# Kernel optimization log

Hardware: AMD Instinct MI355X
Metric: run time of the kernel (lower is better)

The kernel has to match this reference:

```python
import jax, jax.numpy as jnp
import numpy as np

K = 512
D = 512
N_D = 4
SUB_D = D // N_D  # 128
B, T = 16, 2048
TAU = 2.0


def setup_inputs() -> dict:
    key = jax.random.key(0)
    kx, kw1, kw2, kw3, kw4, kg = jax.random.split(key, 6)
    x = jax.random.normal(kx, (B, D, T), dtype=jnp.float32)
    scale = 1.0 / K
    def init_w(k):
        return jax.random.uniform(k, (K, SUB_D), dtype=jnp.float32, minval=-scale, maxval=scale)
    W1, W2, W3, W4 = init_w(kw1), init_w(kw2), init_w(kw3), init_w(kw4)
    # Standard Gumbel noise g = -log(-log(U)), fixed here for reproducibility
    u = jax.random.uniform(kg, (N_D, B * T, K), dtype=jnp.float32, minval=1e-10, maxval=1.0)
    gumbels = -jnp.log(-jnp.log(u))
    return {"x": x, "W1": W1, "W2": W2, "W3": W3, "W4": W4, "gumbels": gumbels}


def reference(x, W1, W2, W3, W4, gumbels):
    # x: [B, D, T] -> [B, T, D] -> flat [N, D] -> [n_d, N, sub_D]
    Bv, Dv, Tv = x.shape
    flat = jnp.transpose(x, (0, 2, 1)).reshape(-1, Dv)          # [N, D]
    xg = jnp.transpose(flat.reshape(-1, N_D, SUB_D), (1, 0, 2))  # [n_d, N, sub_D]
    W = jnp.stack([W1, W2, W3, W4], axis=0)                      # [n_d, K, sub_D]

    code_sqr = jnp.sum(W * W, axis=-1)                           # [n_d, K]
    in_sqr = jnp.sum(xg * xg, axis=-1, keepdims=True)            # [n_d, N, 1]
    cross = jnp.einsum('gnd,gkd->gnk', xg, W)                    # [n_d, N, K]
    dis = code_sqr[:, None, :] + in_sqr - 2.0 * cross            # [n_d, N, K]

    # gumbel_softmax(-dis, tau, hard=False): softmax((logits + g)/tau)
    enc = jax.nn.softmax((-dis + gumbels) / TAU, axis=-1)        # [n_d, N, K]

    quant = jnp.einsum('gnk,gkd->gnd', enc, W)                   # [n_d, N, sub_D]
    quant = jnp.transpose(quant, (1, 0, 2)).reshape(Bv, Tv, Dv)  # concat sub-dims
    quant = jnp.transpose(quant, (0, 2, 1))                      # [B, D, T]

    avg_probs = jnp.mean(enc, axis=1)                            # [n_d, K]
    perp = jnp.sum(jnp.exp(-jnp.sum(avg_probs * jnp.log(avg_probs + 1e-10), axis=-1)))
    return quant, perp
```

## Files before the change

### kernel.cpp

```cpp
#include <hip/hip_runtime.h>
#include <hip/hip_bf16.h>
#include <math.h>

#define K_CODES 512
#define D_FULL 512
#define SUB_D 128
#define N_D 4
#define B_SZ 16
#define T_SZ 2048
#define N_TOK (B_SZ * T_SZ)
#define TILE 32
#define XS_STRIDE 136
#define ENC_STRIDE 520
#define QS_STRIDE 33

typedef __attribute__((ext_vector_type(8))) short short8;
typedef __attribute__((ext_vector_type(16))) float f32x16;

__device__ __forceinline__ unsigned short f2bf(float f) {
    __hip_bfloat16 h = __float2bfloat16(f);
    return *reinterpret_cast<unsigned short*>(&h);
}
__device__ __forceinline__ float bf2f(unsigned short u) {
    unsigned int v = ((unsigned int)u) << 16;
    return __uint_as_float(v);
}

#define XS_OFF  33280
#define RED_OFF 41984
#define SMEM_SZ 42496

__global__ __launch_bounds__(256, 3) void vq_kernel(
    const float* __restrict__ x,
    const unsigned short* __restrict__ Wbf,
    const unsigned short* __restrict__ WTbf,
    const float* __restrict__ csqr,
    const float* __restrict__ gum,
    float* __restrict__ out,
    float* __restrict__ wsum, int Rmask)
{
    __shared__ __align__(16) char smem[SMEM_SZ];
    unsigned short* enc = (unsigned short*)smem;
    unsigned short* xs  = (unsigned short*)(smem + XS_OFF);
    float* Sred = (float*)(smem + RED_OFF);
    float* Qs   = (float*)smem;

    const int tid = threadIdx.x;
    const int g = blockIdx.y;
    const int n0 = blockIdx.x * TILE;
    const int b = n0 / T_SZ;
    const int t0 = n0 % T_SZ;
    const int wave = tid >> 6, lane = tid & 63;
    const int half = lane >> 5, l31 = lane & 31;

    const float* xbase = x + ((size_t)b * D_FULL + g * SUB_D) * T_SZ + t0;
    #pragma unroll
    for (int it = 0; it < 4; ++it) {
        int idx = tid + it * 256;
        int tq = idx & 7, d = idx >> 3;
        float4 v = *(const float4*)(xbase + (size_t)d * T_SZ + tq * 4);
        int t = tq * 4;
        xs[(t + 0) * XS_STRIDE + d] = f2bf(v.x);
        xs[(t + 1) * XS_STRIDE + d] = f2bf(v.y);
        xs[(t + 2) * XS_STRIDE + d] = f2bf(v.z);
        xs[(t + 3) * XS_STRIDE + d] = f2bf(v.w);
    }
    __syncthreads();

    short8 afrag[8];
    #pragma unroll
    for (int s = 0; s < 8; ++s)
        afrag[s] = *(const short8*)(xs + l31 * XS_STRIDE + s * 16 + half * 8);

    float csq[4];
    #pragma unroll
    for (int ct = 0; ct < 4; ++ct)
        csq[ct] = csqr[g * K_CODES + wave * 128 + ct * 32 + l31];

    __syncthreads();

    const unsigned short* Wg = Wbf + (size_t)g * K_CODES * SUB_D;
    f32x16 acc[4];
    #pragma unroll
    for (int ct = 0; ct < 4; ++ct)
        #pragma unroll
        for (int i = 0; i < 16; ++i) acc[ct][i] = 0.f;

    #pragma unroll
    for (int s = 0; s < 8; ++s) {
        #pragma unroll
        for (int ct = 0; ct < 4; ++ct) {
            short8 bfrag = *(const short8*)(Wg + (size_t)(wave * 128 + ct * 32 + l31) * SUB_D
                                            + s * 16 + half * 8);
            acc[ct] = __builtin_amdgcn_mfma_f32_32x32x16_bf16(afrag[s], bfrag, acc[ct], 0, 0, 0);
        }
    }

    __builtin_amdgcn_sched_barrier(0);

    const float* gw = gum + ((size_t)g * N_TOK + n0) * K_CODES + wave * 128;
    float4 f[16];
    #pragma unroll
    for (int k = 0; k < 16; ++k)
        f[k] = *(const float4*)(gw + (size_t)(2 * k + half) * K_CODES + 4 * l31);

    float* Sw = (float*)(smem + XS_OFF) + wave * 544;
    float ssum[16];
    #pragma unroll
    for (int i = 0; i < 16; ++i) ssum[i] = 0.f;

    #pragma unroll
    for (int j = 0; j < 8; ++j) {
        *(float4*)(Sw + half * 128 + 4 * l31)       = f[2 * j];
        *(float4*)(Sw + 256 + half * 128 + 4 * l31) = f[2 * j + 1];
        int hj = j & 1;
        if (half == hj) {
            int q = (j - hj) >> 1;
            #pragma unroll
            for (int ct = 0; ct < 4; ++ct)
                #pragma unroll
                for (int m = 0; m < 4; ++m) {
                    float gv = Sw[m * 128 + ct * 32 + l31];
                    int i = q * 4 + m;
                    float e = __expf(acc[ct][i] - 0.5f * csq[ct] + 0.5f * gv);
                    acc[ct][i] = e;
                    ssum[i] += e;
                }
        }
    }

    #pragma unroll
    for (int i = 0; i < 16; ++i) {
        float s = ssum[i];
        s += __shfl_xor(s, 1);  s += __shfl_xor(s, 2);
        s += __shfl_xor(s, 4);  s += __shfl_xor(s, 8);
        s += __shfl_xor(s, 16);
        ssum[i] = s;
    }
    if (l31 == 0) {
        #pragma unroll
        for (int i = 0; i < 16; ++i)
            Sred[((i & 3) + 8 * (i >> 2) + 4 * half) * 4 + wave] = ssum[i];
    }
    __syncthreads();
    float rinv[16];
    #pragma unroll
    for (int i = 0; i < 16; ++i) {
        int r = (i & 3) + 8 * (i >> 2) + 4 * half;
        float4 sv = *(const float4*)&Sred[r * 4];
        rinv[i] = 1.f / (sv.x + sv.y + sv.z + sv.w);
    }

    float* wrep = wsum + (size_t)(blockIdx.x & Rmask) * (N_D * K_CODES) + g * K_CODES;
    #pragma unroll
    for (int ct = 0; ct < 4; ++ct) {
        float s = 0.f;
        #pragma unroll
        for (int i = 0; i < 16; ++i) {
            int r = (i & 3) + 8 * (i >> 2) + 4 * half;
            float p = acc[ct][i] * rinv[i];
            enc[r * ENC_STRIDE + wave * 128 + ct * 32 + l31] = f2bf(p);
            s += p;
        }
        s += __shfl_xor(s, 32);
        if (half == 0) atomicAdd(wrep + wave * 128 + ct * 32 + l31, s);
    }
    __syncthreads();

    const unsigned short* Btrow = WTbf + (size_t)g * SUB_D * K_CODES
                                + (size_t)(wave * 32 + l31) * K_CODES + half * 8;
    f32x16 q0, q1;
    #pragma unroll
    for (int i = 0; i < 16; ++i) { q0[i] = 0.f; q1[i] = 0.f; }
    #pragma unroll
    for (int s = 0; s < 32; s += 2) {
        short8 a0 = *(const short8*)(enc + l31 * ENC_STRIDE + (s + 0) * 16 + half * 8);
        short8 b0 = *(const short8*)(Btrow + (s + 0) * 16);
        short8 a1 = *(const short8*)(enc + l31 * ENC_STRIDE + (s + 1) * 16 + half * 8);
        short8 b1 = *(const short8*)(Btrow + (s + 1) * 16);
        q0 = __builtin_amdgcn_mfma_f32_32x32x16_bf16(a0, b0, q0, 0, 0, 0);
        q1 = __builtin_amdgcn_mfma_f32_32x32x16_bf16(a1, b1, q1, 0, 0, 0);
    }
    __syncthreads();

    #pragma unroll
    for (int i = 0; i < 16; ++i) {
        int r = (i & 3) + 8 * (i >> 2) + 4 * half;
        Qs[(wave * 32 + l31) * QS_STRIDE + r] = q0[i] + q1[i];
    }
    __syncthreads();

    float* obase = out + ((size_t)b * D_FULL + g * SUB_D) * T_SZ + t0;
    #pragma unroll
    for (int it = 0; it < 4; ++it) {
        int idx = tid + it * 256;
        int t4 = (idx & 7) * 4, j = idx >> 3;
        float4 v;
        v.x = Qs[j * QS_STRIDE + t4 + 0];
        v.y = Qs[j * QS_STRIDE + t4 + 1];
        v.z = Qs[j * QS_STRIDE + t4 + 2];
        v.w = Qs[j * QS_STRIDE + t4 + 3];
        *(float4*)(obase + (size_t)j * T_SZ + t4) = v;
    }
}

__global__ __launch_bounds__(256) void prep_kernel(
    const float* __restrict__ W1, const float* __restrict__ W2,
    const float* __restrict__ W3, const float* __restrict__ W4,
    unsigned short* __restrict__ Wbf, unsigned short* __restrict__ WTbf,
    float* __restrict__ csqr)
{
    const int g = blockIdx.x, kc = blockIdx.y;
    const float* Wg = (g == 0) ? W1 : ((g == 1) ? W2 : ((g == 2) ? W3 : W4));
    const int tid = threadIdx.x;
    const int k0 = kc * 64;
    __shared__ float tile[64][129];

    #pragma unroll
    for (int it = 0; it < 8; ++it) {
        int idx = tid + it * 256;
        int k = idx >> 5, d4 = (idx & 31) * 4;
        float4 v = *(const float4*)(Wg + (size_t)(k0 + k) * SUB_D + d4);
        unsigned short p0 = f2bf(v.x), p1 = f2bf(v.y), p2 = f2bf(v.z), p3 = f2bf(v.w);
        tile[k][d4 + 0] = bf2f(p0); tile[k][d4 + 1] = bf2f(p1);
        tile[k][d4 + 2] = bf2f(p2); tile[k][d4 + 3] = bf2f(p3);
        ushort4 pk; pk.x = p0; pk.y = p1; pk.z = p2; pk.w = p3;
        *(ushort4*)(Wbf + (size_t)g * K_CODES * SUB_D + (size_t)(k0 + k) * SUB_D + d4) = pk;
    }
    __syncthreads();

    #pragma unroll
    for (int it = 0; it < 4; ++it) {
        int idx = tid + it * 256;
        int d = idx >> 3, c8 = (idx & 7) * 8;
        union { unsigned short u[8]; short8 v; } pk;
        #pragma unroll
        for (int j = 0; j < 8; ++j) pk.u[j] = f2bf(tile[c8 + j][d]);
        *(short8*)(WTbf + (size_t)g * SUB_D * K_CODES + (size_t)d * K_CODES + k0 + c8) = pk.v;
    }

    if (tid < 64) {
        float ssq = 0.f;
        #pragma unroll 16
        for (int d = 0; d < SUB_D; ++d) { float wv = tile[tid][d]; ssq += wv * wv; }
        csqr[g * K_CODES + k0 + tid] = ssq;
    }
}

__global__ __launch_bounds__(256) void perp_kernel(
    const float* __restrict__ wsum, int R, float* __restrict__ out)
{
    const int tid = threadIdx.x;
    const int lane = tid & 63, wave = tid >> 6;
    __shared__ float red[N_D][4];
    float part[N_D];
    #pragma unroll
    for (int g = 0; g < N_D; ++g) part[g] = 0.f;

    for (int g = 0; g < N_D; ++g) {
        for (int kk = tid; kk < K_CODES; kk += 256) {
            float s = 0.f;
            for (int r = 0; r < R; ++r) s += wsum[(size_t)r * (N_D * K_CODES) + g * K_CODES + kk];
            float p = s * (1.0f / N_TOK);
            part[g] += p * logf(p + 1e-10f);
        }
    }
    #pragma unroll
    for (int g = 0; g < N_D; ++g) {
        float v = part[g];
        #pragma unroll
        for (int off = 32; off; off >>= 1) v += __shfl_xor(v, off);
        if (lane == 0) red[g][wave] = v;
    }
    __syncthreads();
    if (tid == 0) {
        float perp = 0.f;
        #pragma unroll
        for (int g = 0; g < N_D; ++g) {
            float e = red[g][0] + red[g][1] + red[g][2] + red[g][3];
            perp += __expf(-e);
        }
        out[(size_t)B_SZ * D_FULL * T_SZ] = perp;
    }
}

extern "C" void kernel_launch(void* const* d_in, const int* in_sizes, int n_in,
                              void* d_out, int out_size, void* d_ws, size_t ws_size,
                              hipStream_t stream) {
    const float* x   = (const float*)d_in[0];
    const float* W1  = (const float*)d_in[1];
    const float* W2  = (const float*)d_in[2];
    const float* W3  = (const float*)d_in[3];
    const float* W4  = (const float*)d_in[4];
    const float* gum = (const float*)d_in[5];
    float* out = (float*)d_out;

    unsigned short* Wbf  = (unsigned short*)d_ws;
    unsigned short* WTbf = Wbf + (size_t)N_D * K_CODES * SUB_D;
    float* csqr = (float*)(WTbf + (size_t)N_D * K_CODES * SUB_D);
    float* wsum = csqr + N_D * K_CODES;

    size_t fixed = (size_t)N_D * K_CODES * SUB_D * 2 * 2 + (size_t)N_D * K_CODES * 4;
    size_t rem = (ws_size > fixed) ? (ws_size - fixed) : 0;
    int maxR = (int)(rem / ((size_t)N_D * K_CODES * 4));
    int R = 1;
    while (R * 2 <= maxR && R < 16) R *= 2;

    hipMemsetAsync(wsum, 0, (size_t)R * N_D * K_CODES * sizeof(float), stream);
    prep_kernel<<<dim3(4, 8), 256, 0, stream>>>(W1, W2, W3, W4, Wbf, WTbf, csqr);
    vq_kernel<<<dim3(N_TOK / TILE, N_D), 256, 0, stream>>>(x, Wbf, WTbf, csqr, gum, out, wsum, R - 1);
    perp_kernel<<<1, 256, 0, stream>>>(wsum, R, out);
}
```

Measured before the change: 569.1 us.

## Swizzle shared-memory layouts to drop padding and raise occupancy to four blocks

```diff
diff --git a/kernel.cpp b/kernel.cpp
--- a/kernel.cpp
+++ b/kernel.cpp
@@ -10,8 +10,6 @@
 #define T_SZ 2048
 #define N_TOK (B_SZ * T_SZ)
 #define TILE 32
-#define XS_STRIDE 136
-#define ENC_STRIDE 520
 #define QS_STRIDE 33
 
 typedef __attribute__((ext_vector_type(8))) short short8;
@@ -26,11 +24,13 @@
     return __uint_as_float(v);
 }
 
-#define XS_OFF  33280
-#define RED_OFF 41984
-#define SMEM_SZ 42496
-
-__global__ __launch_bounds__(256, 3) void vq_kernel(
+#define XS_OFF  32768
+#define SMEM_SZ 40960
+
+__device__ __forceinline__ int enc_idx(int r, int c) { return r * 512 + (c ^ ((r & 7) << 3)); }
+__device__ __forceinline__ int xs_idx(int t, int d)  { return t * 128 + (d ^ ((t & 7) << 3)); }
+
+__global__ __launch_bounds__(256, 4) void vq_kernel(
     const float* __restrict__ x,
     const unsigned short* __restrict__ Wbf,
     const unsigned short* __restrict__ WTbf,
@@ -42,7 +42,7 @@
     __shared__ __align__(16) char smem[SMEM_SZ];
     unsigned short* enc = (unsigned short*)smem;
     unsigned short* xs  = (unsigned short*)(smem + XS_OFF);
-    float* Sred = (float*)(smem + RED_OFF);
+    float* Sp   = (float*)smem;
     float* Qs   = (float*)smem;
 
     const int tid = threadIdx.x;
@@ -60,25 +60,18 @@
         int tq = idx & 7, d = idx >> 3;
         float4 v = *(const float4*)(xbase + (size_t)d * T_SZ + tq * 4);
         int t = tq * 4;
-        xs[(t + 0) * XS_STRIDE + d] = f2bf(v.x);
-        xs[(t + 1) * XS_STRIDE + d] = f2bf(v.y);
-        xs[(t + 2) * XS_STRIDE + d] = f2bf(v.z);
-        xs[(t + 3) * XS_STRIDE + d] = f2bf(v.w);
-    }
-    __syncthreads();
-
-    short8 afrag[8];
-    #pragma unroll
-    for (int s = 0; s < 8; ++s)
-        afrag[s] = *(const short8*)(xs + l31 * XS_STRIDE + s * 16 + half * 8);
+        xs[xs_idx(t + 0, d)] = f2bf(v.x);
+        xs[xs_idx(t + 1, d)] = f2bf(v.y);
+        xs[xs_idx(t + 2, d)] = f2bf(v.z);
+        xs[xs_idx(t + 3, d)] = f2bf(v.w);
+    }
+    __syncthreads();
 
     float csq[4];
     #pragma unroll
     for (int ct = 0; ct < 4; ++ct)
         csq[ct] = csqr[g * K_CODES + wave * 128 + ct * 32 + l31];
 
-    __syncthreads();
-
     const unsigned short* Wg = Wbf + (size_t)g * K_CODES * SUB_D;
     f32x16 acc[4];
     #pragma unroll
@@ -88,11 +81,12 @@
 
     #pragma unroll
     for (int s = 0; s < 8; ++s) {
+        short8 af = *(const short8*)(xs + xs_idx(l31, s * 16 + half * 8));
         #pragma unroll
         for (int ct = 0; ct < 4; ++ct) {
             short8 bfrag = *(const short8*)(Wg + (size_t)(wave * 128 + ct * 32 + l31) * SUB_D
                                             + s * 16 + half * 8);
-            acc[ct] = __builtin_amdgcn_mfma_f32_32x32x16_bf16(afrag[s], bfrag, acc[ct], 0, 0, 0);
+            acc[ct] = __builtin_amdgcn_mfma_f32_32x32x16_bf16(af, bfrag, acc[ct], 0, 0, 0);
         }
     }
 
@@ -104,7 +98,7 @@
     for (int k = 0; k < 16; ++k)
         f[k] = *(const float4*)(gw + (size_t)(2 * k + half) * K_CODES + 4 * l31);
 
-    float* Sw = (float*)(smem + XS_OFF) + wave * 544;
+    float* Sw = Sp + wave * 544;
     float ssum[16];
     #pragma unroll
     for (int i = 0; i < 16; ++i) ssum[i] = 0.f;
@@ -140,16 +134,18 @@
     if (l31 == 0) {
         #pragma unroll
         for (int i = 0; i < 16; ++i)
-            Sred[((i & 3) + 8 * (i >> 2) + 4 * half) * 4 + wave] = ssum[i];
-    }
-    __syncthreads();
+            Sw[512 + (i & 3) + 8 * (i >> 2) + 4 * half] = ssum[i];
+    }
+    __syncthreads();
+
     float rinv[16];
     #pragma unroll
     for (int i = 0; i < 16; ++i) {
         int r = (i & 3) + 8 * (i >> 2) + 4 * half;
-        float4 sv = *(const float4*)&Sred[r * 4];
-        rinv[i] = 1.f / (sv.x + sv.y + sv.z + sv.w);
-    }
+        float s = Sp[512 + r] + Sp[544 + 512 + r] + Sp[1088 + 512 + r] + Sp[1632 + 512 + r];
+        rinv[i] = 1.f / s;
+    }
+    __syncthreads();
 
     float* wrep = wsum + (size_t)(blockIdx.x & Rmask) * (N_D * K_CODES) + g * K_CODES;
     #pragma unroll
@@ -159,7 +155,7 @@
         for (int i = 0; i < 16; ++i) {
             int r = (i & 3) + 8 * (i >> 2) + 4 * half;
             float p = acc[ct][i] * rinv[i];
-            enc[r * ENC_STRIDE + wave * 128 + ct * 32 + l31] = f2bf(p);
+            enc[enc_idx(r, wave * 128 + ct * 32 + l31)] = f2bf(p);
             s += p;
         }
         s += __shfl_xor(s, 32);
@@ -174,9 +170,9 @@
     for (int i = 0; i < 16; ++i) { q0[i] = 0.f; q1[i] = 0.f; }
     #pragma unroll
     for (int s = 0; s < 32; s += 2) {
-        short8 a0 = *(const short8*)(enc + l31 * ENC_STRIDE + (s + 0) * 16 + half * 8);
+        short8 a0 = *(const short8*)(enc + enc_idx(l31, (s + 0) * 16 + half * 8));
         short8 b0 = *(const short8*)(Btrow + (s + 0) * 16);
-        short8 a1 = *(const short8*)(enc + l31 * ENC_STRIDE + (s + 1) * 16 + half * 8);
+        short8 a1 = *(const short8*)(enc + enc_idx(l31, (s + 1) * 16 + half * 8));
         short8 b1 = *(const short8*)(Btrow + (s + 1) * 16);
         q0 = __builtin_amdgcn_mfma_f32_32x32x16_bf16(a0, b0, q0, 0, 0, 0);
         q1 = __builtin_amdgcn_mfma_f32_32x32x16_bf16(a1, b1, q1, 0, 0, 0);
```

New measurement: 576.7 us. No clear change (+1.3%).
